# Kernel tuning notes

Measured on AMD Instinct MI355X. Metric: run time of the kernel, lower is better.

## Reference

```python
import jax, jax.numpy as jnp
import numpy as np

N = 100000
E = 3200000
IN_F = 256
OUT_F = 128
ALPHA = 0.2  # LeakyReLU negative slope


def setup_inputs() -> dict:
    key = jax.random.key(0)
    k1, k2, k3, k4, k5 = jax.random.split(key, 5)
    x = jax.random.normal(k1, (N, IN_F), dtype=jnp.float32)
    edge_row = jax.random.randint(k2, (E,), 0, N, dtype=jnp.int32)
    edge_col = jax.random.randint(k3, (E,), 0, N, dtype=jnp.int32)
    # xavier-uniform style scaling (gain 1.414)
    lim_W = 1.414 * np.sqrt(6.0 / (IN_F + OUT_F))
    W = jax.random.uniform(k4, (IN_F, OUT_F), minval=-lim_W, maxval=lim_W, dtype=jnp.float32)
    lim_a = 1.414 * np.sqrt(6.0 / (1 + 2 * OUT_F))
    a = jax.random.uniform(k5, (2 * OUT_F,), minval=-lim_a, maxval=lim_a, dtype=jnp.float32)
    return {"x": x, "edge_row": edge_row, "edge_col": edge_col, "W": W, "a": a}


def reference(x, edge_row, edge_col, W, a):
    # h = x @ W : [N, OUT_F]
    h = x @ W
    # edge score: leakyrelu([h_src || h_dst] . a) computed as two node-level dots
    a_src, a_dst = a[:OUT_F], a[OUT_F:]
    s_src = h @ a_src  # [N]
    s_dst = h @ a_dst  # [N]
    e = s_src[edge_row] + s_dst[edge_col]  # [E]
    e = jnp.where(e > 0, e, ALPHA * e)     # LeakyReLU
    # sparse softmax along dim=1 (over columns within each row -> segment by row)
    row_max = jax.ops.segment_max(e, edge_row, num_segments=N)  # [N]
    e_exp = jnp.exp(e - row_max[edge_row])
    row_sum = jax.ops.segment_sum(e_exp, edge_row, num_segments=N)  # [N]
    att = e_exp / row_sum[edge_row]  # [E]
    # sparse-dense matmul: h_prime[i] = sum_j att_ij * h[j]
    h_prime = jax.ops.segment_sum(att[:, None] * h[edge_col], edge_row, num_segments=N)
    # concat=True -> ELU
    return jax.nn.elu(h_prime)
```

## Files before the change

kernel.cpp:

```cpp
#include <hip/hip_runtime.h>
#include <math.h>

#define N_NODES 100000
#define N_EDGES 3200000
#define IN_FEAT 256
#define OUT_FEAT 128
#define ALPHA 0.2f
#define NB 782
#define NBLK 200
#define CHUNK 16000

#define SCAN_N (NB * NBLK)
#define SCAN_ELEMS 2048
#define SCAN_BLOCKS ((SCAN_N + SCAN_ELEMS - 1) / SCAN_ELEMS)

typedef __attribute__((ext_vector_type(8))) short short8;
typedef __attribute__((ext_vector_type(4))) float f32x4;

__device__ __forceinline__ ushort f2bf(float f) {
  uint u = __float_as_uint(f);
  u = (u + 0x7FFFu + ((u >> 16) & 1u)) >> 16;
  return (ushort)u;
}
__device__ __forceinline__ float bflo(uint u) { return __uint_as_float(u << 16); }
__device__ __forceinline__ float bfhi(uint u) { return __uint_as_float(u & 0xFFFF0000u); }

__global__ __launch_bounds__(256) void wt_kernel(const float* __restrict__ W,
                                                 ushort* __restrict__ Wt) {
  int id = blockIdx.x * 256 + threadIdx.x;
  int c = id >> 8;
  int k = id & 255;
  Wt[id] = f2bf(W[k * OUT_FEAT + c]);
}

#define GBM 128
#define GBK 32
#define A_LD 40
#define C_LD 136

__global__ __launch_bounds__(256) void gemm_h16_kernel(const float* __restrict__ x,
                                                       const ushort* __restrict__ Wt,
                                                       ushort* __restrict__ h16) {
  __shared__ union {
    struct { ushort A[GBM * A_LD]; ushort B[OUT_FEAT * A_LD]; } s;
    ushort C[GBM * C_LD];
  } sm;
  const int tid = threadIdx.x;
  const int row0 = blockIdx.x * GBM;
  const int lane = tid & 63;
  const int wave = tid >> 6;
  const int lr = lane & 15;
  const int lg = lane >> 4;

  f32x4 acc[2][8];
#pragma unroll
  for (int m = 0; m < 2; ++m)
#pragma unroll
    for (int n = 0; n < 8; ++n) acc[m][n] = (f32x4)(0.f);

  const int sr = tid >> 1;
  const int sh = tid & 1;
  const bool arow_ok = (row0 + sr) < N_NODES;
  const float* xg = x + (size_t)(row0 + sr) * IN_FEAT + sh * 16;
  const ushort* wg = Wt + sr * IN_FEAT + sh * 16;

  for (int ks = 0; ks < IN_FEAT / GBK; ++ks) {
    float4 f[4];
    if (arow_ok) {
#pragma unroll
      for (int i = 0; i < 4; ++i) f[i] = *(const float4*)(xg + ks * GBK + i * 4);
    } else {
#pragma unroll
      for (int i = 0; i < 4; ++i) f[i] = make_float4(0.f, 0.f, 0.f, 0.f);
    }
#pragma unroll
    for (int i = 0; i < 4; ++i) {
      uint2 p;
      p.x = (uint)f2bf(f[i].x) | ((uint)f2bf(f[i].y) << 16);
      p.y = (uint)f2bf(f[i].z) | ((uint)f2bf(f[i].w) << 16);
      *(uint2*)&sm.s.A[sr * A_LD + sh * 16 + i * 4] = p;
    }
    {
      short8 b0 = *(const short8*)(wg + ks * GBK);
      short8 b1 = *(const short8*)(wg + ks * GBK + 8);
      *(short8*)&sm.s.B[sr * A_LD + sh * 16] = b0;
      *(short8*)&sm.s.B[sr * A_LD + sh * 16 + 8] = b1;
    }
    __syncthreads();
    short8 af[2], bf[8];
#pragma unroll
    for (int m = 0; m < 2; ++m)
      af[m] = *(const short8*)&sm.s.A[(wave * 32 + m * 16 + lr) * A_LD + lg * 8];
#pragma unroll
    for (int n = 0; n < 8; ++n)
      bf[n] = *(const short8*)&sm.s.B[(n * 16 + lr) * A_LD + lg * 8];
#pragma unroll
    for (int m = 0; m < 2; ++m)
#pragma unroll
      for (int n = 0; n < 8; ++n)
        acc[m][n] = __builtin_amdgcn_mfma_f32_16x16x32_bf16(af[m], bf[n], acc[m][n], 0, 0, 0);
    __syncthreads();
  }

#pragma unroll
  for (int m = 0; m < 2; ++m)
#pragma unroll
    for (int n = 0; n < 8; ++n)
#pragma unroll
      for (int i = 0; i < 4; ++i)
        sm.C[(wave * 32 + m * 16 + lg * 4 + i) * C_LD + n * 16 + lr] = f2bf(acc[m][n][i]);
  __syncthreads();
  {
    int row = tid >> 1;
    if (row0 + row < N_NODES) {
      const ushort* src = &sm.C[row * C_LD + sh * 64];
      ushort* dst = h16 + (size_t)(row0 + row) * OUT_FEAT + sh * 64;
#pragma unroll
      for (int i = 0; i < 8; ++i) *(short8*)(dst + i * 8) = *(const short8*)(src + i * 8);
    }
  }
}

__global__ __launch_bounds__(256) void s16_kernel(const ushort* __restrict__ h16,
                                                  const float* __restrict__ a,
                                                  float* __restrict__ s_src,
                                                  float* __restrict__ s_dst) {
  const int lane = threadIdx.x & 63;
  const int r = blockIdx.x * 4 + (threadIdx.x >> 6);
  uint v = *(const uint*)(h16 + (size_t)r * OUT_FEAT + lane * 2);
  float h0 = bflo(v);
  float h1 = bfhi(v);
  float2 as = *(const float2*)(a + lane * 2);
  float2 ad = *(const float2*)(a + OUT_FEAT + lane * 2);
  float ds = h0 * as.x + h1 * as.y;
  float dd = h0 * ad.x + h1 * ad.y;
#pragma unroll
  for (int off = 32; off >= 1; off >>= 1) {
    ds += __shfl_xor(ds, off, 64);
    dd += __shfl_xor(dd, off, 64);
  }
  if (lane == 0) {
    s_src[r] = ds;
    s_dst[r] = dd;
  }
}

__global__ __launch_bounds__(256) void hist_kernel(const int* __restrict__ erow,
                                                   int* __restrict__ G) {
  __shared__ int hist[NB];
  const int b = blockIdx.x;
  const int t = threadIdx.x;
  for (int k = t; k < NB; k += 256) hist[k] = 0;
  __syncthreads();
  const int base = b * CHUNK;
  for (int i = base + t; i < base + CHUNK; i += 256) atomicAdd(&hist[erow[i] >> 7], 1);
  __syncthreads();
  for (int k = t; k < NB; k += 256) G[k * NBLK + b] = hist[k];
}

__global__ __launch_bounds__(256) void scan1_kernel(const int* __restrict__ src,
                                                    int* __restrict__ dst,
                                                    int* __restrict__ bsum) {
  __shared__ int tsum[256];
  const int b = blockIdx.x;
  const int t = threadIdx.x;
  const int base = b * SCAN_ELEMS + t * 8;
  int v[8];
  int s = 0;
#pragma unroll
  for (int i = 0; i < 8; ++i) {
    int idx = base + i;
    v[i] = (idx < SCAN_N) ? src[idx] : 0;
    s += v[i];
  }
  tsum[t] = s;
  __syncthreads();
  for (int d = 1; d < 256; d <<= 1) {
    int u = (t >= d) ? tsum[t - d] : 0;
    __syncthreads();
    tsum[t] += u;
    __syncthreads();
  }
  int run = (t == 0) ? 0 : tsum[t - 1];
#pragma unroll
  for (int i = 0; i < 8; ++i) {
    int idx = base + i;
    if (idx < SCAN_N) dst[idx] = run;
    run += v[i];
  }
  if (t == 255) bsum[b] = tsum[255];
}

__global__ __launch_bounds__(128) void scan2_kernel(int* __restrict__ bsum,
                                                    int* __restrict__ boff) {
  __shared__ int s[128];
  const int t = threadIdx.x;
  s[t] = (t < SCAN_BLOCKS) ? bsum[t] : 0;
  __syncthreads();
  for (int d = 1; d < 128; d <<= 1) {
    int u = (t >= d) ? s[t - d] : 0;
    __syncthreads();
    s[t] += u;
    __syncthreads();
  }
  boff[t + 1] = s[t];
  if (t == 0) boff[0] = 0;
}

__global__ __launch_bounds__(256) void scan3_kernel(int* __restrict__ dst,
                                                    const int* __restrict__ boff) {
  const int b = blockIdx.x;
  const int t = threadIdx.x;
  const int add = boff[b];
  const int base = b * SCAN_ELEMS + t * 8;
#pragma unroll
  for (int i = 0; i < 8; ++i) {
    int idx = base + i;
    if (idx < SCAN_N) dst[idx] += add;
  }
  if (b == 0 && t == 0) dst[SCAN_N] = boff[SCAN_BLOCKS];
}

__global__ __launch_bounds__(256) void partition_kernel(const int* __restrict__ erow,
                                                        const int* __restrict__ ecol,
                                                        const int* __restrict__ scanG,
                                                        uint* __restrict__ packed) {
  __shared__ int cur[NB];
  const int b = blockIdx.x;
  const int t = threadIdx.x;
  for (int k = t; k < NB; k += 256) cur[k] = scanG[k * NBLK + b];
  __syncthreads();
  const int base = b * CHUNK;
  for (int i = base + t; i < base + CHUNK; i += 256) {
    int r = erow[i];
    int c = ecol[i];
    int pos = atomicAdd(&cur[r >> 7], 1);
    packed[pos] = ((uint)(r & 127) << 17) | (uint)c;
  }
}

__global__ __launch_bounds__(256) void bucket_scatter_kernel(const uint* __restrict__ packed,
                                                             const int* __restrict__ scanG,
                                                             int* __restrict__ offs,
                                                             int* __restrict__ scol) {
  __shared__ int cnt[128];
  __shared__ int sc[128];
  const int b = blockIdx.x;
  const int t = threadIdx.x;
  const int beg = scanG[b * NBLK];
  const int end = scanG[(b + 1) * NBLK];
  if (t < 128) cnt[t] = 0;
  __syncthreads();
  for (int i = beg + t; i < end; i += 256) atomicAdd(&cnt[packed[i] >> 17], 1);
  __syncthreads();
  if (t < 128) sc[t] = cnt[t];
  __syncthreads();
  for (int d = 1; d < 128; d <<= 1) {
    int v = 0;
    if (t >= d && t < 128) v = sc[t - d];
    __syncthreads();
    if (t < 128) sc[t] += v;
    __syncthreads();
  }
  const int row0 = b << 7;
  if (t < 128) {
    int rstart = beg + sc[t] - cnt[t];
    if (row0 + t < N_NODES) offs[row0 + t] = rstart;
    sc[t] = rstart;
    cnt[t] = 0;
  }
  if (b == NB - 1 && t == 0) offs[N_NODES] = end;
  __syncthreads();
  for (int i = beg + t; i < end; i += 256) {
    uint p = packed[i];
    int rl = p >> 17;
    int pos = sc[rl] + atomicAdd(&cnt[rl], 1);
    scol[pos] = (int)(p & 0x1FFFFu);
  }
}

__global__ __launch_bounds__(256) void attn_kernel(const ushort* __restrict__ h16,
                                                   const float* __restrict__ s_src,
                                                   const float* __restrict__ s_dst,
                                                   const int* __restrict__ offs,
                                                   const int* __restrict__ scol,
                                                   float* __restrict__ out) {
  __shared__ uint2 apair[4][128];
  const int lane = threadIdx.x & 63;
  const int w = threadIdx.x >> 6;
  const int r = blockIdx.x * 4 + w;
  const int o0 = offs[r];
  const int deg = offs[r + 1] - o0;
  const int g = lane >> 4;
  const int fo = (lane & 15) * 8;
  float* orow = out + (size_t)r * OUT_FEAT + fo;

  if (deg == 0) {
    if (g == 0) {
      *(float4*)orow = make_float4(0.f, 0.f, 0.f, 0.f);
      *(float4*)(orow + 4) = make_float4(0.f, 0.f, 0.f, 0.f);
    }
    return;
  }

  const float ssrc = s_src[r];
  const ushort* hb = h16 + fo;
  float acc[8] = {0.f, 0.f, 0.f, 0.f, 0.f, 0.f, 0.f, 0.f};

  if (deg <= 128) {
    int c0 = 0, c1 = 0;
    float p0 = -INFINITY, p1 = -INFINITY;
    if (lane < deg) {
      c0 = scol[o0 + lane];
      float e = ssrc + s_dst[c0];
      p0 = e > 0.f ? e : ALPHA * e;
    }
    if (lane + 64 < deg) {
      c1 = scol[o0 + 64 + lane];
      float e = ssrc + s_dst[c1];
      p1 = e > 0.f ? e : ALPHA * e;
    }
    float m = fmaxf(p0, p1);
#pragma unroll
    for (int off = 32; off >= 1; off >>= 1) m = fmaxf(m, __shfl_xor(m, off, 64));
    p0 = __expf(p0 - m);
    p1 = __expf(p1 - m);
    float ssum = p0 + p1;
#pragma unroll
    for (int off = 32; off >= 1; off >>= 1) ssum += __shfl_xor(ssum, off, 64);
    const float inv = 1.f / ssum;
    p0 *= inv;
    p1 *= inv;

    apair[w][lane] = make_uint2(__float_as_uint(p0), (uint)c0);
    apair[w][64 + lane] = make_uint2(__float_as_uint(p1), (uint)c1);

    const int degR = (deg + 3) & ~3;
#pragma unroll 2
    for (int j = 0; j < degR; j += 4) {
      uint2 pr = apair[w][j + g];
      float att = __uint_as_float(pr.x);
      uint4 v = *(const uint4*)(hb + (size_t)pr.y * OUT_FEAT);
      acc[0] = fmaf(att, bflo(v.x), acc[0]);
      acc[1] = fmaf(att, bfhi(v.x), acc[1]);
      acc[2] = fmaf(att, bflo(v.y), acc[2]);
      acc[3] = fmaf(att, bfhi(v.y), acc[3]);
      acc[4] = fmaf(att, bflo(v.z), acc[4]);
      acc[5] = fmaf(att, bfhi(v.z), acc[5]);
      acc[6] = fmaf(att, bflo(v.w), acc[6]);
      acc[7] = fmaf(att, bfhi(v.w), acc[7]);
    }
  } else {
    float m = -INFINITY;
    for (int j = lane; j < deg; j += 64) {
      int c = scol[o0 + j];
      float e = ssrc + s_dst[c];
      e = e > 0.f ? e : ALPHA * e;
      m = fmaxf(m, e);
    }
#pragma unroll
    for (int off = 32; off >= 1; off >>= 1) m = fmaxf(m, __shfl_xor(m, off, 64));
    float ssum = 0.f;
    for (int j = lane; j < deg; j += 64) {
      int c = scol[o0 + j];
      float e = ssrc + s_dst[c];
      e = e > 0.f ? e : ALPHA * e;
      ssum += __expf(e - m);
    }
#pragma unroll
    for (int off = 32; off >= 1; off >>= 1) ssum += __shfl_xor(ssum, off, 64);
    const float inv = 1.f / ssum;
    for (int j = 0; j < deg; j += 4) {
      int jj = j + g;
      float att = 0.f;
      int c = 0;
      if (jj < deg) {
        c = scol[o0 + jj];
        float e = ssrc + s_dst[c];
        e = e > 0.f ? e : ALPHA * e;
        att = __expf(e - m) * inv;
      }
      uint4 v = *(const uint4*)(hb + (size_t)c * OUT_FEAT);
      acc[0] = fmaf(att, bflo(v.x), acc[0]);
      acc[1] = fmaf(att, bfhi(v.x), acc[1]);
      acc[2] = fmaf(att, bflo(v.y), acc[2]);
      acc[3] = fmaf(att, bfhi(v.y), acc[3]);
      acc[4] = fmaf(att, bflo(v.z), acc[4]);
      acc[5] = fmaf(att, bfhi(v.z), acc[5]);
      acc[6] = fmaf(att, bflo(v.w), acc[6]);
      acc[7] = fmaf(att, bfhi(v.w), acc[7]);
    }
  }

#pragma unroll
  for (int k = 0; k < 8; ++k) {
    acc[k] += __shfl_xor(acc[k], 16, 64);
    acc[k] += __shfl_xor(acc[k], 32, 64);
  }
  if (g == 0) {
#pragma unroll
    for (int k = 0; k < 8; ++k) acc[k] = acc[k] > 0.f ? acc[k] : expm1f(acc[k]);
    *(float4*)orow = make_float4(acc[0], acc[1], acc[2], acc[3]);
    *(float4*)(orow + 4) = make_float4(acc[4], acc[5], acc[6], acc[7]);
  }
}

extern "C" void kernel_launch(void* const* d_in, const int* in_sizes, int n_in,
                              void* d_out, int out_size, void* d_ws, size_t ws_size,
                              hipStream_t stream) {
  const float* x = (const float*)d_in[0];
  const int* erow = (const int*)d_in[1];
  const int* ecol = (const int*)d_in[2];
  const float* W = (const float*)d_in[3];
  const float* a = (const float*)d_in[4];
  float* out = (float*)d_out;

  char* ws = (char*)d_ws;
  size_t off = 0;
  auto alloc = [&](size_t bytes) {
    void* p = ws + off;
    off = (off + bytes + 255) & ~(size_t)255;
    return p;
  };
  const int M_PAD = 782 * GBM;
  ushort* h16 = (ushort*)alloc((size_t)M_PAD * OUT_FEAT * sizeof(ushort));
  ushort* Wt = (ushort*)alloc((size_t)IN_FEAT * OUT_FEAT * sizeof(ushort));
  float* s_src = (float*)alloc((size_t)N_NODES * sizeof(float));
  float* s_dst = (float*)alloc((size_t)N_NODES * sizeof(float));
  int* offs = (int*)alloc((size_t)(N_NODES + 1) * sizeof(int));
  int* G = (int*)alloc((size_t)SCAN_N * sizeof(int));
  int* scanG = (int*)alloc((size_t)(SCAN_N + 1) * sizeof(int));
  int* bsum = (int*)alloc((size_t)SCAN_BLOCKS * sizeof(int));
  int* boff = (int*)alloc((size_t)(SCAN_BLOCKS + 64) * sizeof(int));
  uint* packed = (uint*)alloc((size_t)N_EDGES * sizeof(uint));
  int* scol = (int*)alloc((size_t)N_EDGES * sizeof(int));

  wt_kernel<<<(IN_FEAT * OUT_FEAT) / 256, 256, 0, stream>>>(W, Wt);
  gemm_h16_kernel<<<782, 256, 0, stream>>>(x, Wt, h16);
  s16_kernel<<<N_NODES / 4, 256, 0, stream>>>(h16, a, s_src, s_dst);
  hist_kernel<<<NBLK, 256, 0, stream>>>(erow, G);
  scan1_kernel<<<SCAN_BLOCKS, 256, 0, stream>>>(G, scanG, bsum);
  scan2_kernel<<<1, 128, 0, stream>>>(bsum, boff);
  scan3_kernel<<<SCAN_BLOCKS, 256, 0, stream>>>(scanG, boff);
  partition_kernel<<<NBLK, 256, 0, stream>>>(erow, ecol, scanG, packed);
  bucket_scatter_kernel<<<NB, 256, 0, stream>>>(packed, scanG, offs, scol);
  attn_kernel<<<N_NODES / 4, 256, 0, stream>>>(h16, s_src, s_dst, offs, scol, out);
}
```

Before: 242.3 us.

## Fuse attention score dots into GEMM epilogue and enlarge edge-sort block sizes

Measured after the change: 237.2 us. 2.1% less time.

```diff
diff --git a/kernel.cpp b/kernel.cpp
--- a/kernel.cpp
+++ b/kernel.cpp
@@ -40,11 +40,15 @@
 
 __global__ __launch_bounds__(256) void gemm_h16_kernel(const float* __restrict__ x,
                                                        const ushort* __restrict__ Wt,
-                                                       ushort* __restrict__ h16) {
+                                                       const float* __restrict__ a,
+                                                       ushort* __restrict__ h16,
+                                                       float* __restrict__ s_src,
+                                                       float* __restrict__ s_dst) {
   __shared__ union {
     struct { ushort A[GBM * A_LD]; ushort B[OUT_FEAT * A_LD]; } s;
     ushort C[GBM * C_LD];
   } sm;
+  __shared__ float sa[2 * OUT_FEAT];
   const int tid = threadIdx.x;
   const int row0 = blockIdx.x * GBM;
   const int lane = tid & 63;
@@ -52,6 +56,8 @@
   const int lr = lane & 15;
   const int lg = lane >> 4;
 
+  sa[tid] = a[tid];
+
   f32x4 acc[2][8];
 #pragma unroll
   for (int m = 0; m < 2; ++m)
@@ -111,51 +117,43 @@
         sm.C[(wave * 32 + m * 16 + lg * 4 + i) * C_LD + n * 16 + lr] = f2bf(acc[m][n][i]);
   __syncthreads();
   {
-    int row = tid >> 1;
-    if (row0 + row < N_NODES) {
-      const ushort* src = &sm.C[row * C_LD + sh * 64];
+    const int row = sr;
+    const bool ok = (row0 + row) < N_NODES;
+    const ushort* src = &sm.C[row * C_LD + sh * 64];
+    if (ok) {
       ushort* dst = h16 + (size_t)(row0 + row) * OUT_FEAT + sh * 64;
 #pragma unroll
       for (int i = 0; i < 8; ++i) *(short8*)(dst + i * 8) = *(const short8*)(src + i * 8);
     }
-  }
-}
-
-__global__ __launch_bounds__(256) void s16_kernel(const ushort* __restrict__ h16,
-                                                  const float* __restrict__ a,
-                                                  float* __restrict__ s_src,
-                                                  float* __restrict__ s_dst) {
-  const int lane = threadIdx.x & 63;
-  const int r = blockIdx.x * 4 + (threadIdx.x >> 6);
-  uint v = *(const uint*)(h16 + (size_t)r * OUT_FEAT + lane * 2);
-  float h0 = bflo(v);
-  float h1 = bfhi(v);
-  float2 as = *(const float2*)(a + lane * 2);
-  float2 ad = *(const float2*)(a + OUT_FEAT + lane * 2);
-  float ds = h0 * as.x + h1 * as.y;
-  float dd = h0 * ad.x + h1 * ad.y;
-#pragma unroll
-  for (int off = 32; off >= 1; off >>= 1) {
-    ds += __shfl_xor(ds, off, 64);
-    dd += __shfl_xor(dd, off, 64);
-  }
-  if (lane == 0) {
-    s_src[r] = ds;
-    s_dst[r] = dd;
-  }
-}
-
-__global__ __launch_bounds__(256) void hist_kernel(const int* __restrict__ erow,
-                                                   int* __restrict__ G) {
+    float ds = 0.f, dd = 0.f;
+    const float* as = &sa[sh * 64];
+    const float* ad = &sa[OUT_FEAT + sh * 64];
+#pragma unroll
+    for (int i = 0; i < 64; ++i) {
+      float hv = __uint_as_float((uint)src[i] << 16);
+      ds = fmaf(hv, as[i], ds);
+      dd = fmaf(hv, ad[i], dd);
+    }
+    ds += __shfl_xor(ds, 1, 64);
+    dd += __shfl_xor(dd, 1, 64);
+    if (sh == 0 && ok) {
+      s_src[row0 + row] = ds;
+      s_dst[row0 + row] = dd;
+    }
+  }
+}
+
+__global__ __launch_bounds__(1024) void hist_kernel(const int* __restrict__ erow,
+                                                    int* __restrict__ G) {
   __shared__ int hist[NB];
   const int b = blockIdx.x;
   const int t = threadIdx.x;
-  for (int k = t; k < NB; k += 256) hist[k] = 0;
+  for (int k = t; k < NB; k += 1024) hist[k] = 0;
   __syncthreads();
   const int base = b * CHUNK;
-  for (int i = base + t; i < base + CHUNK; i += 256) atomicAdd(&hist[erow[i] >> 7], 1);
-  __syncthreads();
-  for (int k = t; k < NB; k += 256) G[k * NBLK + b] = hist[k];
+  for (int i = base + t; i < base + CHUNK; i += 1024) atomicAdd(&hist[erow[i] >> 7], 1);
+  __syncthreads();
+  for (int k = t; k < NB; k += 1024) G[k * NBLK + b] = hist[k];
 }
 
 __global__ __launch_bounds__(256) void scan1_kernel(const int* __restrict__ src,
@@ -221,17 +219,17 @@
   if (b == 0 && t == 0) dst[SCAN_N] = boff[SCAN_BLOCKS];
 }
 
-__global__ __launch_bounds__(256) void partition_kernel(const int* __restrict__ erow,
-                                                        const int* __restrict__ ecol,
-                                                        const int* __restrict__ scanG,
-                                                        uint* __restrict__ packed) {
+__global__ __launch_bounds__(1024) void partition_kernel(const int* __restrict__ erow,
+                                                         const int* __restrict__ ecol,
+                                                         const int* __restrict__ scanG,
+                                                         uint* __restrict__ packed) {
   __shared__ int cur[NB];
   const int b = blockIdx.x;
   const int t = threadIdx.x;
-  for (int k = t; k < NB; k += 256) cur[k] = scanG[k * NBLK + b];
+  for (int k = t; k < NB; k += 1024) cur[k] = scanG[k * NBLK + b];
   __syncthreads();
   const int base = b * CHUNK;
-  for (int i = base + t; i < base + CHUNK; i += 256) {
+  for (int i = base + t; i < base + CHUNK; i += 1024) {
     int r = erow[i];
     int c = ecol[i];
     int pos = atomicAdd(&cur[r >> 7], 1);
@@ -239,7 +237,7 @@
   }
 }
 
-__global__ __launch_bounds__(256) void bucket_scatter_kernel(const uint* __restrict__ packed,
+__global__ __launch_bounds__(512) void bucket_scatter_kernel(const uint* __restrict__ packed,
                                                              const int* __restrict__ scanG,
                                                              int* __restrict__ offs,
                                                              int* __restrict__ scol) {
@@ -251,7 +249,7 @@
   const int end = scanG[(b + 1) * NBLK];
   if (t < 128) cnt[t] = 0;
   __syncthreads();
-  for (int i = beg + t; i < end; i += 256) atomicAdd(&cnt[packed[i] >> 17], 1);
+  for (int i = beg + t; i < end; i += 512) atomicAdd(&cnt[packed[i] >> 17], 1);
   __syncthreads();
   if (t < 128) sc[t] = cnt[t];
   __syncthreads();
@@ -271,7 +269,7 @@
   }
   if (b == NB - 1 && t == 0) offs[N_NODES] = end;
   __syncthreads();
-  for (int i = beg + t; i < end; i += 256) {
+  for (int i = beg + t; i < end; i += 512) {
     uint p = packed[i];
     int rl = p >> 17;
     int pos = sc[rl] + atomicAdd(&cnt[rl], 1);
@@ -336,7 +334,7 @@
     apair[w][64 + lane] = make_uint2(__float_as_uint(p1), (uint)c1);
 
     const int degR = (deg + 3) & ~3;
-#pragma unroll 2
+#pragma unroll 4
     for (int j = 0; j < degR; j += 4) {
       uint2 pr = apair[w][j + g];
       float att = __uint_as_float(pr.x);
@@ -436,13 +434,12 @@
   int* scol = (int*)alloc((size_t)N_EDGES * sizeof(int));
 
   wt_kernel<<<(IN_FEAT * OUT_FEAT) / 256, 256, 0, stream>>>(W, Wt);
-  gemm_h16_kernel<<<782, 256, 0, stream>>>(x, Wt, h16);
-  s16_kernel<<<N_NODES / 4, 256, 0, stream>>>(h16, a, s_src, s_dst);
-  hist_kernel<<<NBLK, 256, 0, stream>>>(erow, G);
+  gemm_h16_kernel<<<782, 256, 0, stream>>>(x, Wt, a, h16, s_src, s_dst);
+  hist_kernel<<<NBLK, 1024, 0, stream>>>(erow, G);
   scan1_kernel<<<SCAN_BLOCKS, 256, 0, stream>>>(G, scanG, bsum);
   scan2_kernel<<<1, 128, 0, stream>>>(bsum, boff);
   scan3_kernel<<<SCAN_BLOCKS, 256, 0, stream>>>(scanG, boff);
-  partition_kernel<<<NBLK, 256, 0, stream>>>(erow, ecol, scanG, packed);
-  bucket_scatter_kernel<<<NB, 256, 0, stream>>>(packed, scanG, offs, scol);
+  partition_kernel<<<NBLK, 1024, 0, stream>>>(erow, ecol, scanG, packed);
+  bucket_scatter_kernel<<<NB, 512, 0, stream>>>(packed, scanG, offs, scol);
   attn_kernel<<<N_NODES / 4, 256, 0, stream>>>(h16, s_src, s_dst, offs, scol, out);
 }
```
